# Optimization experiments

Hardware: AMD Instinct MI355X
Metric: run time of the kernel (lower is better)

## Reference

```python
import jax, jax.numpy as jnp
import numpy as np

F = 512        # filters (output channels)
C = 512        # input channels
H, W = 256, 256
DENSITY = 26214 / (F * C)  # ~0.1 nonzero fraction (sparsity ~0.9)


def setup_inputs() -> dict:
    key = jax.random.key(0)
    k1, k2, k3, k4 = jax.random.split(key, 4)
    inputs = jax.random.normal(k1, (1, C, H, W), dtype=jnp.float32)
    kernel_vals = jax.random.normal(k2, (F, C), dtype=jnp.float32)
    mask = jax.random.uniform(k3, (F, C)) < DENSITY  # uniform-sparsity connector
    kernel = jnp.where(mask, kernel_vals, 0.0)       # sparse kernel stored dense
    bias = jax.random.normal(k4, (F,), dtype=jnp.float32)
    return {"inputs": inputs, "kernel": kernel, "mask": mask, "bias": bias}


def reference(inputs, kernel, mask, bias):
    # 1x1 conv as spmm: flatten spatial dims -> [C, H*W], sparse kernel [F, C].
    _, c, h, w = inputs.shape
    flat_inputs = inputs.reshape(c, h * w)
    kernel_sp = jnp.where(mask, kernel, 0.0)
    # fused_spmm path: spmm + bias + relu
    flat_output = jax.nn.relu(kernel_sp @ flat_inputs + bias[:, None])
    return flat_output.reshape(1, -1, h, w)
```

## Files before the change

kernel.cpp:

```cpp
#include <hip/hip_runtime.h>
#include <stdint.h>


#define NF 512
#define NC 512
#define HW 65536
#define BN 64

typedef _Float16 f16x8 __attribute__((ext_vector_type(8)));
typedef _Float16 f16x4 __attribute__((ext_vector_type(4)));
typedef float f32x4 __attribute__((ext_vector_type(4)));

__global__ __launch_bounds__(256) void prep_w(const float* __restrict__ kern,
                                              _Float16* __restrict__ wh) {
  const int i = blockIdx.x * 256 + threadIdx.x;
  const float4 v = ((const float4*)kern)[i];
  f16x4 o;
  o[0] = (_Float16)v.x;
  o[1] = (_Float16)v.y;
  o[2] = (_Float16)v.z;
  o[3] = (_Float16)v.w;
  ((f16x4*)wh)[i] = o;
}

__global__ __launch_bounds__(512, 4) void spmm_mfma(
    const float* __restrict__ X, const _Float16* __restrict__ Wh,
    const float* __restrict__ bias, float* __restrict__ out) {
  __shared__ __align__(16) _Float16 xt[BN * NC];

  const int tid = threadIdx.x;
  const int wave = tid >> 6;
  const int lane = tid & 63;
  const int hw0 = blockIdx.x * BN;

  {
    const float* xp = X + hw0 + lane;
    char* rowb = (char*)xt + lane * (NC * 2);
    const int xr = lane & 31;
#pragma unroll
    for (int j = 0; j < 8; ++j) {
      const int c0 = wave * 64 + j * 8;
      f16x8 p;
#pragma unroll
      for (int u = 0; u < 8; ++u) p[u] = (_Float16)xp[(size_t)(c0 + u) * HW];
      *(f16x8*)(rowb + ((((c0 >> 3) ^ xr)) << 4)) = p;
    }
  }
  __syncthreads();

  const int ln = lane & 15;
  const int l4 = lane >> 4;
  const int mrow0 = wave * 64;

  const _Float16* aptr = Wh + (size_t)(mrow0 + ln) * NC + l4 * 8;

  int bbase[4], bxor[4];
#pragma unroll
  for (int nt = 0; nt < 4; ++nt) {
    const int n = nt * 16 + ln;
    bbase[nt] = n * (NC * 2);
    bxor[nt] = n & 31;
  }

  f32x4 acc[4][4] = {};

#pragma unroll 2
  for (int ks = 0; ks < 16; ++ks) {
    f16x8 a[4], b[4];
#pragma unroll
    for (int mt = 0; mt < 4; ++mt)
      a[mt] = *(const f16x8*)(aptr + (size_t)mt * 16 * NC + ks * 32);
#pragma unroll
    for (int nt = 0; nt < 4; ++nt) {
      const int slot = (ks * 4 + l4) ^ bxor[nt];
      b[nt] = *(const f16x8*)((char*)xt + bbase[nt] + (slot << 4));
    }
#pragma unroll
    for (int nt = 0; nt < 4; ++nt)
#pragma unroll
      for (int mt = 0; mt < 4; ++mt)
        acc[mt][nt] = __builtin_amdgcn_mfma_f32_16x16x32_f16(
            a[mt], b[nt], acc[mt][nt], 0, 0, 0);
  }

#pragma unroll
  for (int mt = 0; mt < 4; ++mt) {
#pragma unroll
    for (int r = 0; r < 4; ++r) {
      const int f = mrow0 + mt * 16 + l4 * 4 + r;
      const float bv = bias[f];
      float* op = out + (size_t)f * HW + hw0 + ln;
#pragma unroll
      for (int nt = 0; nt < 4; ++nt)
        op[nt * 16] = fmaxf(acc[mt][nt][r] + bv, 0.f);
    }
  }
}

extern "C" void kernel_launch(void* const* d_in, const int* in_sizes, int n_in,
                              void* d_out, int out_size, void* d_ws, size_t ws_size,
                              hipStream_t stream) {
  const float* X = (const float*)d_in[0];
  const float* kern = (const float*)d_in[1];
  const float* bias = (const float*)d_in[3];
  float* out = (float*)d_out;

  _Float16* wh = (_Float16*)d_ws;

  prep_w<<<NF * NC / 4 / 256, 256, 0, stream>>>(kern, wh);
  spmm_mfma<<<HW / BN, 512, 0, stream>>>(X, wh, bias, out);
}
```

Baseline: 286.9 us.

## Pre-pack weights in MFMA fragment order and pipeline two X tiles per block

Weights are pre-packed into per-lane MFMA fragment order, so each A load is a contiguous coalesced 16-byte read. The block grows to 1024 threads split as 8 M-waves by 2 N-waves and handles two 64-column tiles. The second tile's X values are prefetched into registers while the first tile is computed, which hides global load latency behind MFMA work. The cost is higher register pressure from the 32-float hold buffer plus an extra pair of barriers, and launch_bounds(1024,8) may force register spills.

```diff
diff --git a/kernel.cpp b/kernel.cpp
--- a/kernel.cpp
+++ b/kernel.cpp
@@ -8,38 +8,92 @@
 #define BN 64
 
 typedef _Float16 f16x8 __attribute__((ext_vector_type(8)));
-typedef _Float16 f16x4 __attribute__((ext_vector_type(4)));
 typedef float f32x4 __attribute__((ext_vector_type(4)));
 
 __global__ __launch_bounds__(256) void prep_w(const float* __restrict__ kern,
-                                              _Float16* __restrict__ wh) {
-  const int i = blockIdx.x * 256 + threadIdx.x;
-  const float4 v = ((const float4*)kern)[i];
-  f16x4 o;
-  o[0] = (_Float16)v.x;
-  o[1] = (_Float16)v.y;
-  o[2] = (_Float16)v.z;
-  o[3] = (_Float16)v.w;
-  ((f16x4*)wh)[i] = o;
+                                              _Float16* __restrict__ wpk) {
+  const int idx = blockIdx.x * 256 + threadIdx.x;
+  const int lane = idx & 63;
+  const int ks = (idx >> 6) & 15;
+  const int t = idx >> 10;
+  const int row = t * 16 + (lane & 15);
+  const int col = ks * 32 + (lane >> 4) * 8;
+  const float4 v0 = *(const float4*)(kern + (size_t)row * NC + col);
+  const float4 v1 = *(const float4*)(kern + (size_t)row * NC + col + 4);
+  f16x8 o;
+  o[0] = (_Float16)v0.x; o[1] = (_Float16)v0.y;
+  o[2] = (_Float16)v0.z; o[3] = (_Float16)v0.w;
+  o[4] = (_Float16)v1.x; o[5] = (_Float16)v1.y;
+  o[6] = (_Float16)v1.z; o[7] = (_Float16)v1.w;
+  *(f16x8*)(wpk + (size_t)idx * 8) = o;
 }
 
-__global__ __launch_bounds__(512, 4) void spmm_mfma(
-    const float* __restrict__ X, const _Float16* __restrict__ Wh,
+__device__ __forceinline__ void compute_half(const _Float16* __restrict__ ap,
+                                             const _Float16* __restrict__ bufp,
+                                             int bb0, int bb1, int bx0, int bx1,
+                                             int l4, int ks0, f32x4 acc[4][2]) {
+#pragma unroll
+  for (int kk = 0; kk < 8; ++kk) {
+    const int ks = ks0 + kk;
+    f16x8 a[4], b[2];
+#pragma unroll
+    for (int mt = 0; mt < 4; ++mt)
+      a[mt] = *(const f16x8*)(ap + mt * 8192 + ks * 512);
+    b[0] = *(const f16x8*)((const char*)bufp + bb0 + (((ks * 4 + l4) ^ bx0) << 4));
+    b[1] = *(const f16x8*)((const char*)bufp + bb1 + (((ks * 4 + l4) ^ bx1) << 4));
+#pragma unroll
+    for (int nt = 0; nt < 2; ++nt)
+#pragma unroll
+      for (int mt = 0; mt < 4; ++mt)
+        acc[mt][nt] = __builtin_amdgcn_mfma_f32_16x16x32_f16(a[mt], b[nt],
+                                                             acc[mt][nt], 0, 0, 0);
+  }
+}
+
+__device__ __forceinline__ void epilogue(const f32x4 acc[4][2],
+                                         const float* __restrict__ bias,
+                                         float* __restrict__ out, int f0,
+                                         int col0) {
+#pragma unroll
+  for (int mt = 0; mt < 4; ++mt) {
+#pragma unroll
+    for (int r = 0; r < 4; ++r) {
+      const int f = f0 + mt * 16 + r;
+      const float bv = bias[f];
+      float* op = out + (size_t)f * HW + col0;
+      op[0] = fmaxf(acc[mt][0][r] + bv, 0.f);
+      op[16] = fmaxf(acc[mt][1][r] + bv, 0.f);
+    }
+  }
+}
+
+__global__ __launch_bounds__(1024, 8) void spmm_mfma(
+    const float* __restrict__ X, const _Float16* __restrict__ Wpk,
     const float* __restrict__ bias, float* __restrict__ out) {
   __shared__ __align__(16) _Float16 xt[BN * NC];
 
   const int tid = threadIdx.x;
   const int wave = tid >> 6;
   const int lane = tid & 63;
-  const int hw0 = blockIdx.x * BN;
+  const int ln = lane & 15, l4 = lane >> 4;
+  const int wm = wave & 7, wn = wave >> 3;
+  const int hwb = blockIdx.x * (2 * BN);
+  const int xr = lane & 31;
+
+  const int n0 = wn * 32 + ln;
+  const int bb0 = n0 * (NC * 2);
+  const int bb1 = (n0 + 16) * (NC * 2);
+  const int bx0 = n0 & 31;
+  const int bx1 = (n0 + 16) & 31;
+
+  const _Float16* ap = Wpk + (size_t)wm * 32768 + (size_t)lane * 8;
 
   {
-    const float* xp = X + hw0 + lane;
+    const float* xp = X + hwb + lane;
     char* rowb = (char*)xt + lane * (NC * 2);
-    const int xr = lane & 31;
 #pragma unroll
-    for (int j = 0; j < 8; ++j) {
-      const int c0 = wave * 64 + j * 8;
+    for (int j = 0; j < 4; ++j) {
+      const int c0 = wave * 32 + j * 8;
       f16x8 p;
 #pragma unroll
       for (int u = 0; u < 8; ++u) p[u] = (_Float16)xp[(size_t)(c0 + u) * HW];
@@ -48,53 +102,45 @@
   }
   __syncthreads();
 
-  const int ln = lane & 15;
-  const int l4 = lane >> 4;
-  const int mrow0 = wave * 64;
+  f32x4 acc[4][2] = {};
 
-  const _Float16* aptr = Wh + (size_t)(mrow0 + ln) * NC + l4 * 8;
+  const float* xp1 = X + hwb + BN + lane;
+  float hold[32];
+#pragma unroll
+  for (int u = 0; u < 16; ++u) hold[u] = xp1[(size_t)(wave * 32 + u) * HW];
 
-  int bbase[4], bxor[4];
-#pragma unroll
-  for (int nt = 0; nt < 4; ++nt) {
-    const int n = nt * 16 + ln;
-    bbase[nt] = n * (NC * 2);
-    bxor[nt] = n & 31;
-  }
-
-  f32x4 acc[4][4] = {};
-
-#pragma unroll 2
-  for (int ks = 0; ks < 16; ++ks) {
-    f16x8 a[4], b[4];
-#pragma unroll
-    for (int mt = 0; mt < 4; ++mt)
-      a[mt] = *(const f16x8*)(aptr + (size_t)mt * 16 * NC + ks * 32);
-#pragma unroll
-    for (int nt = 0; nt < 4; ++nt) {
-      const int slot = (ks * 4 + l4) ^ bxor[nt];
-      b[nt] = *(const f16x8*)((char*)xt + bbase[nt] + (slot << 4));
-    }
-#pragma unroll
-    for (int nt = 0; nt < 4; ++nt)
-#pragma unroll
-      for (int mt = 0; mt < 4; ++mt)
-        acc[mt][nt] = __builtin_amdgcn_mfma_f32_16x16x32_f16(
-            a[mt], b[nt], acc[mt][nt], 0, 0, 0);
-  }
+  compute_half(ap, xt, bb0, bb1, bx0, bx1, l4, 0, acc);
 
 #pragma unroll
-  for (int mt = 0; mt < 4; ++mt) {
+  for (int u = 16; u < 32; ++u) hold[u] = xp1[(size_t)(wave * 32 + u) * HW];
+
+  compute_half(ap, xt, bb0, bb1, bx0, bx1, l4, 8, acc);
+
+  epilogue(acc, bias, out, wm * 64 + l4 * 4, hwb + wn * 32 + ln);
+
+  __syncthreads();
+
+  {
+    char* rowb = (char*)xt + lane * (NC * 2);
 #pragma unroll
-    for (int r = 0; r < 4; ++r) {
-      const int f = mrow0 + mt * 16 + l4 * 4 + r;
-      const float bv = bias[f];
-      float* op = out + (size_t)f * HW + hw0 + ln;
+    for (int j = 0; j < 4; ++j) {
+      const int c0 = wave * 32 + j * 8;
+      f16x8 p;
 #pragma unroll
-      for (int nt = 0; nt < 4; ++nt)
-        op[nt * 16] = fmaxf(acc[mt][nt][r] + bv, 0.f);
+      for (int u = 0; u < 8; ++u) p[u] = (_Float16)hold[j * 8 + u];
+      *(f16x8*)(rowb + ((((c0 >> 3) ^ xr)) << 4)) = p;
     }
   }
+  __syncthreads();
+
+#pragma unroll
+  for (int mt = 0; mt < 4; ++mt)
+#pragma unroll
+    for (int nt = 0; nt < 2; ++nt) acc[mt][nt] = (f32x4){0.f, 0.f, 0.f, 0.f};
+
+  compute_half(ap, xt, bb0, bb1, bx0, bx1, l4, 0, acc);
+  compute_half(ap, xt, bb0, bb1, bx0, bx1, l4, 8, acc);
+  epilogue(acc, bias, out, wm * 64 + l4 * 4, hwb + BN + wn * 32 + ln);
 }
 
 extern "C" void kernel_launch(void* const* d_in, const int* in_sizes, int n_in,
@@ -105,8 +151,8 @@
   const float* bias = (const float*)d_in[3];
   float* out = (float*)d_out;
 
-  _Float16* wh = (_Float16*)d_ws;
+  _Float16* wpk = (_Float16*)d_ws;
 
-  prep_w<<<NF * NC / 4 / 256, 256, 0, stream>>>(kern, wh);
-  spmm_mfma<<<HW / BN, 512, 0, stream>>>(X, wh, bias, out);
+  prep_w<<<NF * NC / 8 / 256, 256, 0, stream>>>(kern, wpk);
+  spmm_mfma<<<HW / (2 * BN), 1024, 0, stream>>>(X, wpk, bias, out);
 }
```

Measured after the change: 638.8 us. 2.23x slower.
